# Performance work log

Hardware: AMD Instinct MI355X
Metric: run time of the kernel (lower is better)

## Reference

```python
import jax, jax.numpy as jnp
import numpy as np

B, N, D, H, MLP_H = 4, 2048, 256, 8, 1024
E = 262144
DH = D // H
EPS = 1e-5

def _ln(x, g, b):
    mu = jnp.mean(x, axis=-1, keepdims=True)
    var = jnp.mean((x - mu) ** 2, axis=-1, keepdims=True)
    return (x - mu) * jax.lax.rsqrt(var + EPS) * g + b

def setup_inputs() -> dict:
    key = jax.random.key(0)
    ks = jax.random.split(key, 16)
    s = 0.02
    return {
        "x": jax.random.normal(ks[0], (B, N, D), jnp.float32),
        "edge_index": jax.random.randint(ks[1], (2, E), 0, B * N, dtype=jnp.int64),
        "gc_w": jax.random.normal(ks[2], (D, D), jnp.float32) * s,
        "gc_b": jnp.zeros((D,), jnp.float32),
        "g_gamma": jnp.ones((D,), jnp.float32), "g_beta": jnp.zeros((D,), jnp.float32),
        "wq": jax.random.normal(ks[3], (D, D), jnp.float32) * s, "bq": jnp.zeros((D,), jnp.float32),
        "wk": jax.random.normal(ks[4], (D, D), jnp.float32) * s, "bk": jnp.zeros((D,), jnp.float32),
        "wv": jax.random.normal(ks[5], (D, D), jnp.float32) * s, "bv": jnp.zeros((D,), jnp.float32),
        "wo": jax.random.normal(ks[6], (D, D), jnp.float32) * s, "bo": jnp.zeros((D,), jnp.float32),
        "a_gamma": jnp.ones((D,), jnp.float32), "a_beta": jnp.zeros((D,), jnp.float32),
        "w1": jax.random.normal(ks[7], (D, MLP_H), jnp.float32) * s, "b1": jnp.zeros((MLP_H,), jnp.float32),
        "w2": jax.random.normal(ks[8], (MLP_H, D), jnp.float32) * s, "b2": jnp.zeros((D,), jnp.float32),
        "m_gamma": jnp.ones((D,), jnp.float32), "m_beta": jnp.zeros((D,), jnp.float32),
    }

def reference(x, edge_index, gc_w, gc_b, g_gamma, g_beta,
              wq, bq, wk, bk, wv, bv, wo, bo, a_gamma, a_beta,
              w1, b1, w2, b2, m_gamma, m_beta):
    BN = B * N
    row, col = edge_index[0], edge_index[1]
    # GraphConvolution with symmetric degree normalization
    xf = x.reshape(BN, D)
    xt = xf @ gc_w  # [BN, D]
    deg = jax.ops.segment_sum(jnp.ones((E,), x.dtype), row, num_segments=BN)
    dis = jnp.where(deg > 0, deg ** -0.5, 0.0)  # deg^-0.5, inf -> 0
    norm = dis[row] * dis[col]  # [E]
    out = jax.ops.segment_sum(norm[:, None] * xt[row], col, num_segments=BN) + gc_b
    x = _ln(x + out.reshape(B, N, D), g_gamma, g_beta)
    # Multi-head self-attention (no mask, dropout=0)
    q = (x @ wq + bq).reshape(B, N, H, DH)
    k = (x @ wk + bk).reshape(B, N, H, DH)
    v = (x @ wv + bv).reshape(B, N, H, DH)
    scores = jnp.einsum("bqhd,bkhd->bhqk", q, k) / jnp.sqrt(jnp.float32(DH))
    attn = jax.nn.softmax(scores, axis=-1)
    ao = jnp.einsum("bhqk,bkhd->bqhd", attn, v).reshape(B, N, D) @ wo + bo
    x = _ln(x + ao, a_gamma, a_beta)
    # MLP (GELU exact, dropout inactive at eval)
    h = jax.nn.gelu(x @ w1 + b1, approximate=False)
    x = _ln(x + (h @ w2 + b2), m_gamma, m_beta)
    return x
```

## Files before the change

kernel.cpp:

```cpp
#include <hip/hip_runtime.h>
#include <math.h>

#define Bb 4
#define Nn 2048
#define Dd 256
#define Hh 8
#define DHh 32
#define MLPH 1024
#define Ee 262144
#define BNr 8192
#define KS_S 40
#define VT_S 72

typedef __attribute__((ext_vector_type(8))) short bf8;
typedef __attribute__((ext_vector_type(4))) short s4v;
typedef __attribute__((ext_vector_type(4))) float f4;

__device__ __forceinline__ float gelu_f(float x){
  return 0.5f * x * (1.0f + erff(x * 0.70710678118654752f));
}

__device__ __forceinline__ ushort f2bf(float f){
  union { float f; unsigned u; } v; v.f = f;
  unsigned r = v.u + 0x7fffu + ((v.u >> 16) & 1u);
  return (ushort)(r >> 16);
}
__device__ __forceinline__ float bf2f(ushort u){
  return __uint_as_float((unsigned)u << 16);
}

__global__ void detect_kernel(const int* __restrict__ ei, int* flag){
  __shared__ int nz;
  if (threadIdx.x == 0) nz = 0;
  __syncthreads();
  int any = 0;
  for (int i = threadIdx.x; i < 2048; i += 256)
    if (ei[2*i + 1] != 0) any = 1;
  if (any) atomicOr(&nz, 1);
  __syncthreads();
  if (threadIdx.x == 0) *flag = nz ? 0 : 1;
}

__global__ void count_kernel(const int* __restrict__ ei, const int* __restrict__ flag,
                             int* cnt_row, int* cnt_col){
  int e = blockIdx.x * 256 + threadIdx.x;
  if (e >= Ee) return;
  int m = *flag;
  int r = m ? ei[2*e]          : ei[e];
  int c = m ? ei[2*(Ee + e)]   : ei[Ee + e];
  atomicAdd(&cnt_row[r], 1);
  atomicAdd(&cnt_col[c], 1);
}

__global__ void scan_kernel(const int* __restrict__ cnt, const int* __restrict__ cnt_row,
                            int* start, int* cursor, float* dis){
  __shared__ int part[256];
  int t = threadIdx.x;
  int s = 0;
  for (int i = 0; i < 32; i++) s += cnt[t*32 + i];
  part[t] = s;
  __syncthreads();
  if (t == 0){
    int run = 0;
    for (int i = 0; i < 256; i++){ int tmp = part[i]; part[i] = run; run += tmp; }
    start[BNr] = run;
  }
  __syncthreads();
  int base = part[t];
  for (int i = 0; i < 32; i++){
    start[t*32 + i]  = base;
    cursor[t*32 + i] = base;
    base += cnt[t*32 + i];
  }
  for (int i = t; i < BNr; i += 256){
    int d = cnt_row[i];
    dis[i] = d > 0 ? 1.0f / sqrtf((float)d) : 0.0f;
  }
}

__global__ void fill_kernel(const int* __restrict__ ei, const int* __restrict__ flag,
                            const float* __restrict__ dis,
                            int* cursor, int2* bucket){
  int e = blockIdx.x * 256 + threadIdx.x;
  if (e >= Ee) return;
  int m = *flag;
  int r = m ? ei[2*e]        : ei[e];
  int c = m ? ei[2*(Ee + e)] : ei[Ee + e];
  int p = atomicAdd(&cursor[c], 1);
  int2 pk;
  pk.x = r;
  pk.y = __float_as_int(dis[r] * dis[c]);
  bucket[p] = pk;
}

__device__ __forceinline__ void tconv_body(const float* src, ushort* dst, int R, int C){
  __shared__ float tile[32][33];
  int c0 = blockIdx.x * 32, r0 = blockIdx.y * 32;
  int tx = threadIdx.x & 31, ty = threadIdx.x >> 5;
  for (int i = ty; i < 32; i += 8)
    tile[i][tx] = src[(size_t)(r0 + i) * C + c0 + tx];
  __syncthreads();
  for (int i = ty; i < 32; i += 8)
    dst[(size_t)(c0 + i) * R + r0 + tx] = f2bf(tile[tx][i]);
}

__global__ void tconv_kernel(const float* __restrict__ src, ushort* __restrict__ dst, int R, int C){
  tconv_body(src, dst, R, C);
}

__global__ void tconv5_kernel(const float* s0, const float* s1, const float* s2,
                              const float* s3, const float* s4,
                              ushort* d0, ushort* d1, ushort* d2, ushort* d3, ushort* d4){
  const float* s; ushort* d;
  switch (blockIdx.z){
    case 0: s = s0; d = d0; break;
    case 1: s = s1; d = d1; break;
    case 2: s = s2; d = d2; break;
    case 3: s = s3; d = d3; break;
    default: s = s4; d = d4; break;
  }
  tconv_body(s, d, 256, 256);
}

__global__ void bias_cat_kernel(const float* __restrict__ bq, const float* __restrict__ bk,
                                const float* __restrict__ bv, float* __restrict__ o){
  int i = blockIdx.x * 256 + threadIdx.x;
  if (i < 256) o[i] = bq[i];
  else if (i < 512) o[i] = bk[i - 256];
  else if (i < 768) o[i] = bv[i - 512];
}

__global__ __launch_bounds__(256) void gather_ln_kernel(
    const ushort* __restrict__ xtb, const int2* __restrict__ bucket,
    const int* __restrict__ start,
    const float* __restrict__ x, const float* __restrict__ gc_b,
    const float* __restrict__ gamma, const float* __restrict__ beta,
    float* __restrict__ out, ushort* __restrict__ outb){
  int v = blockIdx.x, t = threadIdx.x;
  int s0 = start[v], s1 = start[v+1];
  float acc = 0.f;
  int ii = s0;
  for (; ii + 3 < s1; ii += 4){
    int2 e0 = bucket[ii],   e1 = bucket[ii+1];
    int2 e2 = bucket[ii+2], e3 = bucket[ii+3];
    float v0 = bf2f(xtb[(size_t)e0.x*Dd + t]);
    float v1 = bf2f(xtb[(size_t)e1.x*Dd + t]);
    float v2 = bf2f(xtb[(size_t)e2.x*Dd + t]);
    float v3 = bf2f(xtb[(size_t)e3.x*Dd + t]);
    acc += __int_as_float(e0.y) * v0 + __int_as_float(e1.y) * v1;
    acc += __int_as_float(e2.y) * v2 + __int_as_float(e3.y) * v3;
  }
  for (; ii < s1; ii++){
    int2 e = bucket[ii];
    acc += __int_as_float(e.y) * bf2f(xtb[(size_t)e.x*Dd + t]);
  }
  float val = x[(size_t)v*Dd + t] + acc + gc_b[t];

  float s = val, s2 = val*val;
  #pragma unroll
  for (int o = 32; o > 0; o >>= 1){ s += __shfl_xor(s, o); s2 += __shfl_xor(s2, o); }
  __shared__ float wsA[4], wsB[4];
  int wid = t >> 6, lane = t & 63;
  if (lane == 0){ wsA[wid] = s; wsB[wid] = s2; }
  __syncthreads();
  float mu = (wsA[0]+wsA[1]+wsA[2]+wsA[3]) * (1.0f/Dd);
  float ms = (wsB[0]+wsB[1]+wsB[2]+wsB[3]) * (1.0f/Dd);
  float var = ms - mu*mu;
  float res = (val - mu) * rsqrtf(var + 1e-5f) * gamma[t] + beta[t];
  out[(size_t)v*Dd + t] = res;
  outb[(size_t)v*Dd + t] = f2bf(res);
}

__global__ __launch_bounds__(256) void add_ln_kernel(
    const float* __restrict__ a, const float* __restrict__ b,
    const float* __restrict__ gamma, const float* __restrict__ beta,
    float* __restrict__ out, ushort* __restrict__ outb){
  int row = blockIdx.x, t = threadIdx.x;
  size_t off = (size_t)row*Dd + t;
  float val = a[off] + b[off];

  float s = val, s2 = val*val;
  #pragma unroll
  for (int o = 32; o > 0; o >>= 1){ s += __shfl_xor(s, o); s2 += __shfl_xor(s2, o); }
  __shared__ float wsA[4], wsB[4];
  int wid = t >> 6, lane = t & 63;
  if (lane == 0){ wsA[wid] = s; wsB[wid] = s2; }
  __syncthreads();
  float mu = (wsA[0]+wsA[1]+wsA[2]+wsA[3]) * (1.0f/Dd);
  float ms = (wsB[0]+wsB[1]+wsB[2]+wsB[3]) * (1.0f/Dd);
  float var = ms - mu*mu;
  float res = (val - mu) * rsqrtf(var + 1e-5f) * gamma[t] + beta[t];
  out[off] = res;
  if (outb) outb[off] = f2bf(res);
}

#define LDA_S 56

template<int EPI>
__global__ __launch_bounds__(256,2) void gemm_bf16(
    const ushort* __restrict__ A, const ushort* __restrict__ Bt,
    const float* __restrict__ bias, float* __restrict__ Cf, ushort* __restrict__ Cb,
    int M, int K, int N, float qscale,
    ushort* __restrict__ Qp, ushort* __restrict__ Kp, ushort* __restrict__ VtG){
  __shared__ ushort As[2][128*LDA_S];
  __shared__ ushort Bs[2][64*LDA_S];
  int t = threadIdx.x;
  int lane = t & 63, wid = t >> 6;
  int wm = wid >> 1, wn = wid & 1;
  int l15 = lane & 15, lg = lane >> 4;
  int m0 = blockIdx.y * 128, n0 = blockIdx.x * 64;

  int sr = t >> 2;
  int sk = (t & 3) * 8;
  const ushort* Ag1 = A  + (size_t)(m0 + sr) * K + sk;
  const ushort* Ag2 = A  + (size_t)(m0 + 64 + sr) * K + sk;
  const ushort* Bg  = Bt + (size_t)(n0 + sr) * K + sk;

  int nsteps = K / 32;
  bf8 ra1 = *(const bf8*)Ag1;
  bf8 ra2 = *(const bf8*)Ag2;
  bf8 rb  = *(const bf8*)Bg;
  *(bf8*)&As[0][sr*LDA_S + sk]        = ra1;
  *(bf8*)&As[0][(64+sr)*LDA_S + sk]   = ra2;
  *(bf8*)&Bs[0][sr*LDA_S + sk]        = rb;
  __syncthreads();

  f4 acc[4][2] = {};
  for (int ks = 0; ks < nsteps; ks++){
    int cur = ks & 1;
    if (ks + 1 < nsteps){
      ra1 = *(const bf8*)(Ag1 + (ks+1)*32);
      ra2 = *(const bf8*)(Ag2 + (ks+1)*32);
      rb  = *(const bf8*)(Bg  + (ks+1)*32);
    }
    bf8 af[4], bfr[2];
    #pragma unroll
    for (int mf = 0; mf < 4; mf++)
      af[mf] = *(bf8*)&As[cur][(wm*64 + mf*16 + l15)*LDA_S + lg*8];
    #pragma unroll
    for (int nf = 0; nf < 2; nf++)
      bfr[nf] = *(bf8*)&Bs[cur][(wn*32 + nf*16 + l15)*LDA_S + lg*8];
    #pragma unroll
    for (int mf = 0; mf < 4; mf++)
      #pragma unroll
      for (int nf = 0; nf < 2; nf++)
        acc[mf][nf] = __builtin_amdgcn_mfma_f32_16x16x32_bf16(af[mf], bfr[nf], acc[mf][nf], 0, 0, 0);
    __syncthreads();
    if (ks + 1 < nsteps){
      int nxt = cur ^ 1;
      *(bf8*)&As[nxt][sr*LDA_S + sk]      = ra1;
      *(bf8*)&As[nxt][(64+sr)*LDA_S + sk] = ra2;
      *(bf8*)&Bs[nxt][sr*LDA_S + sk]      = rb;
      __syncthreads();
    }
  }

  #pragma unroll
  for (int mf = 0; mf < 4; mf++){
    int row = m0 + wm*64 + mf*16 + lg*4;
    #pragma unroll
    for (int nf = 0; nf < 2; nf++){
      int col = n0 + wn*32 + nf*16 + l15;
      float bv = bias ? bias[col] : 0.f;
      float vv[4];
      #pragma unroll
      for (int r = 0; r < 4; r++) vv[r] = acc[mf][nf][r] + bv;
      if (EPI == 0){
        #pragma unroll
        for (int r = 0; r < 4; r++) Cf[(size_t)(row + r) * N + col] = vv[r];
      } else if (EPI == 2){
        #pragma unroll
        for (int r = 0; r < 4; r++) Cb[(size_t)(row + r) * N + col] = f2bf(gelu_f(vv[r]));
      } else {
        if (n0 < 256){
          #pragma unroll
          for (int r = 0; r < 4; r++)
            Qp[(size_t)(row + r) * Dd + col] = f2bf(vv[r] * qscale);
        } else if (n0 < 512){
          int h = (col - 256) >> 5, dh = (col - 256) & 31;
          int bb = row >> 11, n = row & 2047;
          #pragma unroll
          for (int r = 0; r < 4; r++)
            Kp[((size_t)(bb*Hh + h)*Nn + n + r)*DHh + dh] = f2bf(vv[r]);
        } else {
          int h = (col - 512) >> 5, dh = (col - 512) & 31;
          int bb = row >> 11, n = row & 2047;
          ushort4 pk;
          pk.x = f2bf(vv[0]); pk.y = f2bf(vv[1]);
          pk.z = f2bf(vv[2]); pk.w = f2bf(vv[3]);
          *(ushort4*)&VtG[((size_t)(bb*Hh + h)*DHh + dh)*Nn + n] = pk;
        }
      }
    }
  }
}

template<int OB, int AF>
__global__ __launch_bounds__(256,4) void gemm64_bf16(
    const void* __restrict__ Av, const ushort* __restrict__ Bt,
    const float* __restrict__ bias, float* __restrict__ Cf, ushort* __restrict__ Cb,
    int M, int K, int N){
  __shared__ ushort As[2][64*LDA_S];
  __shared__ ushort Bs[2][64*LDA_S];
  int t = threadIdx.x;
  int lane = t & 63, wid = t >> 6;
  int wm = wid >> 1, wn = wid & 1;
  int l15 = lane & 15, lg = lane >> 4;
  int m0 = blockIdx.y * 64, n0 = blockIdx.x * 64;
  int sr = t >> 2, sk = (t & 3) * 8;
  const ushort* Ag = (const ushort*)Av + (size_t)(m0 + sr) * K + sk;
  const float*  Af = (const float*)Av  + (size_t)(m0 + sr) * K + sk;
  const ushort* Bg = Bt + (size_t)(n0 + sr) * K + sk;
  int nsteps = K / 32;

  bf8 ra; float4 rf0, rf1;
  if (AF){ rf0 = *(const float4*)Af; rf1 = *(const float4*)(Af + 4); }
  else   { ra = *(const bf8*)Ag; }
  bf8 rb = *(const bf8*)Bg;
  if (AF){
    bf8 c;
    c[0]=(short)f2bf(rf0.x); c[1]=(short)f2bf(rf0.y); c[2]=(short)f2bf(rf0.z); c[3]=(short)f2bf(rf0.w);
    c[4]=(short)f2bf(rf1.x); c[5]=(short)f2bf(rf1.y); c[6]=(short)f2bf(rf1.z); c[7]=(short)f2bf(rf1.w);
    *(bf8*)&As[0][sr*LDA_S + sk] = c;
  } else {
    *(bf8*)&As[0][sr*LDA_S + sk] = ra;
  }
  *(bf8*)&Bs[0][sr*LDA_S + sk] = rb;
  __syncthreads();

  f4 acc[2][2] = {};
  for (int ks = 0; ks < nsteps; ks++){
    int cur = ks & 1;
    if (ks + 1 < nsteps){
      if (AF){ rf0 = *(const float4*)(Af + (ks+1)*32); rf1 = *(const float4*)(Af + (ks+1)*32 + 4); }
      else   { ra = *(const bf8*)(Ag + (ks+1)*32); }
      rb = *(const bf8*)(Bg + (ks+1)*32);
    }
    bf8 af[2], bfr[2];
    #pragma unroll
    for (int mf = 0; mf < 2; mf++)
      af[mf] = *(bf8*)&As[cur][(wm*32 + mf*16 + l15)*LDA_S + lg*8];
    #pragma unroll
    for (int nf = 0; nf < 2; nf++)
      bfr[nf] = *(bf8*)&Bs[cur][(wn*32 + nf*16 + l15)*LDA_S + lg*8];
    #pragma unroll
    for (int mf = 0; mf < 2; mf++)
      #pragma unroll
      for (int nf = 0; nf < 2; nf++)
        acc[mf][nf] = __builtin_amdgcn_mfma_f32_16x16x32_bf16(af[mf], bfr[nf], acc[mf][nf], 0, 0, 0);
    __syncthreads();
    if (ks + 1 < nsteps){
      int nxt = cur ^ 1;
      if (AF){
        bf8 c;
        c[0]=(short)f2bf(rf0.x); c[1]=(short)f2bf(rf0.y); c[2]=(short)f2bf(rf0.z); c[3]=(short)f2bf(rf0.w);
        c[4]=(short)f2bf(rf1.x); c[5]=(short)f2bf(rf1.y); c[6]=(short)f2bf(rf1.z); c[7]=(short)f2bf(rf1.w);
        *(bf8*)&As[nxt][sr*LDA_S + sk] = c;
      } else {
        *(bf8*)&As[nxt][sr*LDA_S + sk] = ra;
      }
      *(bf8*)&Bs[nxt][sr*LDA_S + sk] = rb;
      __syncthreads();
    }
  }
  #pragma unroll
  for (int mf = 0; mf < 2; mf++){
    int row = m0 + wm*32 + mf*16 + lg*4;
    #pragma unroll
    for (int nf = 0; nf < 2; nf++){
      int col = n0 + wn*32 + nf*16 + l15;
      float bv = bias ? bias[col] : 0.f;
      #pragma unroll
      for (int r = 0; r < 4; r++){
        float v = acc[mf][nf][r] + bv;
        if (OB) Cb[(size_t)(row + r) * N + col] = f2bf(v);
        else    Cf[(size_t)(row + r) * N + col] = v;
      }
    }
  }
}

__global__ __launch_bounds__(256,4) void attn5_kernel(
    const ushort* __restrict__ Qp, const ushort* __restrict__ Kp,
    const ushort* __restrict__ VtG, ushort* __restrict__ AO){
  __shared__ ushort Ks[2][64*KS_S];
  __shared__ ushort Vt[2][32*VT_S];
  int bh = blockIdx.x >> 5, qb = blockIdx.x & 31;
  int b = bh >> 3, h = bh & 7;
  const ushort* Kh = Kp  + (size_t)bh*Nn*DHh;
  const ushort* Vh = VtG + (size_t)bh*DHh*Nn;
  int t = threadIdx.x;
  int lane = t & 63, wid = t >> 6;
  int l15 = lane & 15, lg = lane >> 4;
  int q0 = qb*64 + wid*16;

  bf8 qf = *(const bf8*)&Qp[(size_t)(b*Nn + q0 + l15)*Dd + h*DHh + lg*8];

  int krow = t >> 2, kc8 = (t & 3) * 8;
  int vrow = t >> 3, vc8 = (t & 7) * 8;
  const ushort* Kg = Kh + (size_t)krow*DHh + kc8;
  const ushort* Vg = Vh + (size_t)vrow*Nn + vc8;

  bf8 kreg = *(const bf8*)Kg;
  bf8 vreg = *(const bf8*)Vg;
  *(bf8*)&Ks[0][krow*KS_S + kc8] = kreg;
  *(bf8*)&Vt[0][vrow*VT_S + vc8] = vreg;
  __syncthreads();

  float m_st = -1e30f, l_st = 0.f;
  f4 oacc[2] = {};

  const int NT = Nn/64;
  for (int kc = 0; kc < NT; kc++){
    int cur = kc & 1;
    if (kc + 1 < NT){
      kreg = *(const bf8*)(Kg + (size_t)(kc+1)*64*DHh);
      vreg = *(const bf8*)(Vg + (kc+1)*64);
    }

    f4 s[4] = {};
    #pragma unroll
    for (int kt = 0; kt < 4; kt++){
      bf8 kf = *(bf8*)&Ks[cur][(kt*16 + l15)*KS_S + lg*8];
      s[kt] = __builtin_amdgcn_mfma_f32_16x16x32_bf16(kf, qf, s[kt], 0, 0, 0);
    }

    float mx = s[0][0];
    #pragma unroll
    for (int kt = 0; kt < 4; kt++)
      #pragma unroll
      for (int r = 0; r < 4; r++)
        mx = fmaxf(mx, s[kt][r]);
    if (__any(mx > m_st + 11.0f)){
      float mw = fmaxf(mx, __shfl_xor(mx, 16));
      mw = fmaxf(mw, __shfl_xor(mw, 32));
      float Mn = fmaxf(m_st, mw);
      float corr = exp2f(m_st - Mn);
      l_st *= corr;
      #pragma unroll
      for (int r = 0; r < 4; r++){
        float cr = __shfl(corr, (lane & 48) | (lg*4 + r));
        oacc[0][r] *= cr;
        oacc[1][r] *= cr;
      }
      m_st = Mn;
    }

    s4v pa[4];
    float ps = 0.f;
    #pragma unroll
    for (int kt = 0; kt < 4; kt++){
      unsigned pb[4];
      #pragma unroll
      for (int r = 0; r < 4; r++){
        float p = exp2f(s[kt][r] - m_st);
        pb[r] = __float_as_uint(p) & 0xffff0000u;
        ps += __uint_as_float(pb[r]);
      }
      union { unsigned u[2]; s4v v; } cvt;
      cvt.u[0] = (pb[0] >> 16) | pb[1];
      cvt.u[1] = (pb[2] >> 16) | pb[3];
      pa[kt] = cvt.v;
    }
    ps += __shfl_xor(ps, 16);
    ps += __shfl_xor(ps, 32);
    l_st += ps;

    #pragma unroll
    for (int kt = 0; kt < 4; kt++)
      #pragma unroll
      for (int nt = 0; nt < 2; nt++){
        s4v vf = *(const s4v*)&Vt[cur][(nt*16 + l15)*VT_S + kt*16 + lg*4];
        oacc[nt] = __builtin_amdgcn_mfma_f32_16x16x16bf16_1k(pa[kt], vf, oacc[nt], 0, 0, 0);
      }

    if (kc + 1 < NT){
      *(bf8*)&Ks[cur^1][krow*KS_S + kc8] = kreg;
      *(bf8*)&Vt[cur^1][vrow*VT_S + vc8] = vreg;
    }
    __syncthreads();
  }

  float l = l_st;
  l += __shfl_xor(l, 16);
  l += __shfl_xor(l, 32);
  float invl = 1.0f / l;
  #pragma unroll
  for (int r = 0; r < 4; r++){
    float il = __shfl(invl, (lane & 48) | (lg*4 + r));
    int row = b*Nn + q0 + lg*4 + r;
    #pragma unroll
    for (int nt = 0; nt < 2; nt++)
      AO[(size_t)row*Dd + h*DHh + nt*16 + l15] = f2bf(oacc[nt][r] * il);
  }
}

extern "C" void kernel_launch(void* const* d_in, const int* in_sizes, int n_in,
                              void* d_out, int out_size, void* d_ws, size_t ws_size,
                              hipStream_t stream){
  const float* x      = (const float*)d_in[0];
  const int*   ei     = (const int*)d_in[1];
  const float* gc_w   = (const float*)d_in[2];
  const float* gc_b   = (const float*)d_in[3];
  const float* g_gamma= (const float*)d_in[4];
  const float* g_beta = (const float*)d_in[5];
  const float* wq = (const float*)d_in[6];  const float* bq = (const float*)d_in[7];
  const float* wk = (const float*)d_in[8];  const float* bk = (const float*)d_in[9];
  const float* wv = (const float*)d_in[10]; const float* bv = (const float*)d_in[11];
  const float* wo = (const float*)d_in[12]; const float* bo = (const float*)d_in[13];
  const float* a_gamma = (const float*)d_in[14]; const float* a_beta = (const float*)d_in[15];
  const float* w1 = (const float*)d_in[16]; const float* b1 = (const float*)d_in[17];
  const float* w2 = (const float*)d_in[18]; const float* b2 = (const float*)d_in[19];
  const float* m_gamma = (const float*)d_in[20]; const float* m_beta = (const float*)d_in[21];
  float* out = (float*)d_out;

  const size_t S = (size_t)BNr * Dd;

  char* p = (char*)d_ws;
  auto alloc = [&](size_t bytes){ char* r = p; p += (bytes + 255) & ~(size_t)255; return r; };

  float* X1    = (float*)alloc(S * 4);
  float* X2    = (float*)alloc(S * 4);
  float* MO    = (float*)alloc(S * 4);
  float* PROJ  = (float*)alloc(S * 4);
  ushort* Qp   = (ushort*)alloc(S * 2);
  ushort* Kp   = (ushort*)alloc(S * 2);
  ushort* VtG  = (ushort*)alloc(S * 2);
  ushort* regA = (ushort*)alloc(S * 2);
  ushort* XTb  = (ushort*)alloc(S * 2);
  ushort* X1b  = (ushort*)alloc(S * 2);
  ushort* Hb   = (ushort*)alloc((size_t)BNr * MLPH * 2);
  ushort* gcwT = (ushort*)alloc(65536 * 2);
  ushort* wqkvT= (ushort*)alloc(196608 * 2);
  ushort* woT  = (ushort*)alloc(65536 * 2);
  ushort* w1T  = (ushort*)alloc(262144 * 2);
  ushort* w2T  = (ushort*)alloc(262144 * 2);
  float* bqkv  = (float*)alloc(768 * 4);
  int* cnt_row = (int*)alloc(8192 * 4);
  int* cnt_col = (int*)alloc(8192 * 4);
  int* startA  = (int*)alloc(8200 * 4);
  int* cursor  = (int*)alloc(8192 * 4);
  int2* bucket = (int2*)alloc(Ee * 8);
  float* dis   = (float*)alloc(8192 * 4);
  int* flag    = (int*)alloc(256);

  ushort* AOb = regA;
  ushort* X2b = XTb;

  hipMemsetAsync(cnt_row, 0, 2 * 8192 * sizeof(int), stream);

  detect_kernel<<<1, 256, 0, stream>>>(ei, flag);
  count_kernel<<<Ee/256, 256, 0, stream>>>(ei, flag, cnt_row, cnt_col);
  scan_kernel<<<1, 256, 0, stream>>>(cnt_col, cnt_row, startA, cursor, dis);
  fill_kernel<<<Ee/256, 256, 0, stream>>>(ei, flag, dis, cursor, bucket);

  tconv5_kernel<<<dim3(8,8,5), 256, 0, stream>>>(gc_w, wq, wk, wv, wo,
      gcwT, wqkvT, wqkvT + 65536, wqkvT + 131072, woT);
  tconv_kernel<<<dim3(32,8), 256, 0, stream>>>(w1, w1T, 256, 1024);
  tconv_kernel<<<dim3(8,32), 256, 0, stream>>>(w2, w2T, 1024, 256);
  bias_cat_kernel<<<3, 256, 0, stream>>>(bq, bk, bv, bqkv);

  const float qscale = 0.17677669529663687f * 1.4426950408889634f;

  gemm64_bf16<1,1><<<dim3(Dd/64, BNr/64), 256, 0, stream>>>(
      x, gcwT, nullptr, nullptr, XTb, BNr, Dd, Dd);
  gather_ln_kernel<<<BNr, 256, 0, stream>>>(XTb, bucket, startA,
                                            x, gc_b, g_gamma, g_beta, X1, X1b);
  gemm_bf16<3><<<dim3(768/64, BNr/128), 256, 0, stream>>>(
      X1b, wqkvT, bqkv, nullptr, nullptr, BNr, Dd, 768, qscale, Qp, Kp, VtG);
  attn5_kernel<<<Bb*Hh*32, 256, 0, stream>>>(Qp, Kp, VtG, AOb);
  gemm64_bf16<0,0><<<dim3(Dd/64, BNr/64), 256, 0, stream>>>(
      AOb, woT, bo, PROJ, nullptr, BNr, Dd, Dd);
  add_ln_kernel<<<BNr, 256, 0, stream>>>(X1, PROJ, a_gamma, a_beta, X2, X2b);
  gemm_bf16<2><<<dim3(MLPH/64, BNr/128), 256, 0, stream>>>(
      X2b, w1T, b1, nullptr, Hb, BNr, Dd, MLPH, 1.0f, nullptr, nullptr, nullptr);
  gemm64_bf16<0,0><<<dim3(Dd/64, BNr/64), 256, 0, stream>>>(
      Hb, w2T, b2, MO, nullptr, BNr, MLPH, Dd);
  add_ln_kernel<<<BNr, 256, 0, stream>>>(X2, MO, m_gamma, m_beta, out, nullptr);
}
```

Before: 341.6 us.

## Double K-step depth in GEMMs and key tile size in attention

Both GEMM kernels now stage 64-wide K slices in shared memory instead of 32, which halves the number of barrier pairs and lets each thread issue more loads per step. The attention kernel processes 128 keys per iteration instead of 64, so online-softmax rescaling and synchronisation happen half as often. It also drops the per-iteration cross-lane reduction of the row sum and defers it to the end. The cost is more shared memory and registers, which may lower occupancy.

```diff
diff --git a/kernel.cpp b/kernel.cpp
--- a/kernel.cpp
+++ b/kernel.cpp
@@ -9,8 +9,9 @@
 #define MLPH 1024
 #define Ee 262144
 #define BNr 8192
-#define KS_S 40
-#define VT_S 72
+#define KS2 40
+#define VS2 136
+#define LDB 72
 
 typedef __attribute__((ext_vector_type(8))) short bf8;
 typedef __attribute__((ext_vector_type(4))) short s4v;
@@ -194,63 +195,69 @@
   if (outb) outb[off] = f2bf(res);
 }
 
-#define LDA_S 56
-
 template<int EPI>
 __global__ __launch_bounds__(256,2) void gemm_bf16(
     const ushort* __restrict__ A, const ushort* __restrict__ Bt,
     const float* __restrict__ bias, float* __restrict__ Cf, ushort* __restrict__ Cb,
     int M, int K, int N, float qscale,
     ushort* __restrict__ Qp, ushort* __restrict__ Kp, ushort* __restrict__ VtG){
-  __shared__ ushort As[2][128*LDA_S];
-  __shared__ ushort Bs[2][64*LDA_S];
+  __shared__ ushort As[2][128*LDB];
+  __shared__ ushort Bs[2][64*LDB];
   int t = threadIdx.x;
   int lane = t & 63, wid = t >> 6;
   int wm = wid >> 1, wn = wid & 1;
   int l15 = lane & 15, lg = lane >> 4;
   int m0 = blockIdx.y * 128, n0 = blockIdx.x * 64;
 
-  int sr = t >> 2;
-  int sk = (t & 3) * 8;
-  const ushort* Ag1 = A  + (size_t)(m0 + sr) * K + sk;
-  const ushort* Ag2 = A  + (size_t)(m0 + 64 + sr) * K + sk;
-  const ushort* Bg  = Bt + (size_t)(n0 + sr) * K + sk;
-
-  int nsteps = K / 32;
-  bf8 ra1 = *(const bf8*)Ag1;
-  bf8 ra2 = *(const bf8*)Ag2;
-  bf8 rb  = *(const bf8*)Bg;
-  *(bf8*)&As[0][sr*LDA_S + sk]        = ra1;
-  *(bf8*)&As[0][(64+sr)*LDA_S + sk]   = ra2;
-  *(bf8*)&Bs[0][sr*LDA_S + sk]        = rb;
+  int ar = t >> 1, ac = (t & 1) * 32;
+  int br = t >> 2, bc = (t & 3) * 16;
+  const ushort* Ag = A  + (size_t)(m0 + ar) * K + ac;
+  const ushort* Bg = Bt + (size_t)(n0 + br) * K + bc;
+
+  int nsteps = K / 64;
+  bf8 a0 = *(const bf8*)(Ag + 0),  a1 = *(const bf8*)(Ag + 8);
+  bf8 a2 = *(const bf8*)(Ag + 16), a3 = *(const bf8*)(Ag + 24);
+  bf8 b0 = *(const bf8*)(Bg + 0),  b1r = *(const bf8*)(Bg + 8);
+  *(bf8*)&As[0][ar*LDB + ac + 0]  = a0;
+  *(bf8*)&As[0][ar*LDB + ac + 8]  = a1;
+  *(bf8*)&As[0][ar*LDB + ac + 16] = a2;
+  *(bf8*)&As[0][ar*LDB + ac + 24] = a3;
+  *(bf8*)&Bs[0][br*LDB + bc + 0]  = b0;
+  *(bf8*)&Bs[0][br*LDB + bc + 8]  = b1r;
   __syncthreads();
 
   f4 acc[4][2] = {};
   for (int ks = 0; ks < nsteps; ks++){
     int cur = ks & 1;
     if (ks + 1 < nsteps){
-      ra1 = *(const bf8*)(Ag1 + (ks+1)*32);
-      ra2 = *(const bf8*)(Ag2 + (ks+1)*32);
-      rb  = *(const bf8*)(Bg  + (ks+1)*32);
-    }
-    bf8 af[4], bfr[2];
-    #pragma unroll
-    for (int mf = 0; mf < 4; mf++)
-      af[mf] = *(bf8*)&As[cur][(wm*64 + mf*16 + l15)*LDA_S + lg*8];
-    #pragma unroll
-    for (int nf = 0; nf < 2; nf++)
-      bfr[nf] = *(bf8*)&Bs[cur][(wn*32 + nf*16 + l15)*LDA_S + lg*8];
-    #pragma unroll
-    for (int mf = 0; mf < 4; mf++)
+      a0 = *(const bf8*)(Ag + (ks+1)*64 + 0);  a1 = *(const bf8*)(Ag + (ks+1)*64 + 8);
+      a2 = *(const bf8*)(Ag + (ks+1)*64 + 16); a3 = *(const bf8*)(Ag + (ks+1)*64 + 24);
+      b0 = *(const bf8*)(Bg + (ks+1)*64 + 0);  b1r = *(const bf8*)(Bg + (ks+1)*64 + 8);
+    }
+    #pragma unroll
+    for (int kk = 0; kk < 2; kk++){
+      bf8 af[4], bfr[2];
+      #pragma unroll
+      for (int mf = 0; mf < 4; mf++)
+        af[mf] = *(bf8*)&As[cur][(wm*64 + mf*16 + l15)*LDB + kk*32 + lg*8];
       #pragma unroll
       for (int nf = 0; nf < 2; nf++)
-        acc[mf][nf] = __builtin_amdgcn_mfma_f32_16x16x32_bf16(af[mf], bfr[nf], acc[mf][nf], 0, 0, 0);
+        bfr[nf] = *(bf8*)&Bs[cur][(wn*32 + nf*16 + l15)*LDB + kk*32 + lg*8];
+      #pragma unroll
+      for (int mf = 0; mf < 4; mf++)
+        #pragma unroll
+        for (int nf = 0; nf < 2; nf++)
+          acc[mf][nf] = __builtin_amdgcn_mfma_f32_16x16x32_bf16(af[mf], bfr[nf], acc[mf][nf], 0, 0, 0);
+    }
     __syncthreads();
     if (ks + 1 < nsteps){
       int nxt = cur ^ 1;
-      *(bf8*)&As[nxt][sr*LDA_S + sk]      = ra1;
-      *(bf8*)&As[nxt][(64+sr)*LDA_S + sk] = ra2;
-      *(bf8*)&Bs[nxt][sr*LDA_S + sk]      = rb;
+      *(bf8*)&As[nxt][ar*LDB + ac + 0]  = a0;
+      *(bf8*)&As[nxt][ar*LDB + ac + 8]  = a1;
+      *(bf8*)&As[nxt][ar*LDB + ac + 16] = a2;
+      *(bf8*)&As[nxt][ar*LDB + ac + 24] = a3;
+      *(bf8*)&Bs[nxt][br*LDB + bc + 0]  = b0;
+      *(bf8*)&Bs[nxt][br*LDB + bc + 8]  = b1r;
       __syncthreads();
     }
   }
@@ -300,66 +307,82 @@
     const void* __restrict__ Av, const ushort* __restrict__ Bt,
     const float* __restrict__ bias, float* __restrict__ Cf, ushort* __restrict__ Cb,
     int M, int K, int N){
-  __shared__ ushort As[2][64*LDA_S];
-  __shared__ ushort Bs[2][64*LDA_S];
+  __shared__ ushort As[2][64*LDB];
+  __shared__ ushort Bs[2][64*LDB];
   int t = threadIdx.x;
   int lane = t & 63, wid = t >> 6;
   int wm = wid >> 1, wn = wid & 1;
   int l15 = lane & 15, lg = lane >> 4;
   int m0 = blockIdx.y * 64, n0 = blockIdx.x * 64;
-  int sr = t >> 2, sk = (t & 3) * 8;
-  const ushort* Ag = (const ushort*)Av + (size_t)(m0 + sr) * K + sk;
-  const float*  Af = (const float*)Av  + (size_t)(m0 + sr) * K + sk;
-  const ushort* Bg = Bt + (size_t)(n0 + sr) * K + sk;
-  int nsteps = K / 32;
-
-  bf8 ra; float4 rf0, rf1;
-  if (AF){ rf0 = *(const float4*)Af; rf1 = *(const float4*)(Af + 4); }
-  else   { ra = *(const bf8*)Ag; }
-  bf8 rb = *(const bf8*)Bg;
+  int ar = t >> 2, ac = (t & 3) * 16;
+  const ushort* Ag = (const ushort*)Av + (size_t)(m0 + ar) * K + ac;
+  const float*  Af = (const float*)Av  + (size_t)(m0 + ar) * K + ac;
+  const ushort* Bg = Bt + (size_t)(n0 + ar) * K + ac;
+  int nsteps = K / 64;
+
+  bf8 a0, a1, b0, b1r;
+  float4 rf0, rf1, rf2, rf3;
   if (AF){
-    bf8 c;
-    c[0]=(short)f2bf(rf0.x); c[1]=(short)f2bf(rf0.y); c[2]=(short)f2bf(rf0.z); c[3]=(short)f2bf(rf0.w);
-    c[4]=(short)f2bf(rf1.x); c[5]=(short)f2bf(rf1.y); c[6]=(short)f2bf(rf1.z); c[7]=(short)f2bf(rf1.w);
-    *(bf8*)&As[0][sr*LDA_S + sk] = c;
+    rf0 = *(const float4*)(Af + 0);  rf1 = *(const float4*)(Af + 4);
+    rf2 = *(const float4*)(Af + 8);  rf3 = *(const float4*)(Af + 12);
+    bf8 c0, c1;
+    c0[0]=(short)f2bf(rf0.x); c0[1]=(short)f2bf(rf0.y); c0[2]=(short)f2bf(rf0.z); c0[3]=(short)f2bf(rf0.w);
+    c0[4]=(short)f2bf(rf1.x); c0[5]=(short)f2bf(rf1.y); c0[6]=(short)f2bf(rf1.z); c0[7]=(short)f2bf(rf1.w);
+    c1[0]=(short)f2bf(rf2.x); c1[1]=(short)f2bf(rf2.y); c1[2]=(short)f2bf(rf2.z); c1[3]=(short)f2bf(rf2.w);
+    c1[4]=(short)f2bf(rf3.x); c1[5]=(short)f2bf(rf3.y); c1[6]=(short)f2bf(rf3.z); c1[7]=(short)f2bf(rf3.w);
+    a0 = c0; a1 = c1;
   } else {
-    *(bf8*)&As[0][sr*LDA_S + sk] = ra;
-  }
-  *(bf8*)&Bs[0][sr*LDA_S + sk] = rb;
+    a0 = *(const bf8*)(Ag + 0); a1 = *(const bf8*)(Ag + 8);
+  }
+  b0 = *(const bf8*)(Bg + 0); b1r = *(const bf8*)(Bg + 8);
+  *(bf8*)&As[0][ar*LDB + ac + 0] = a0;
+  *(bf8*)&As[0][ar*LDB + ac + 8] = a1;
+  *(bf8*)&Bs[0][ar*LDB + ac + 0] = b0;
+  *(bf8*)&Bs[0][ar*LDB + ac + 8] = b1r;
   __syncthreads();
 
   f4 acc[2][2] = {};
   for (int ks = 0; ks < nsteps; ks++){
     int cur = ks & 1;
     if (ks + 1 < nsteps){
-      if (AF){ rf0 = *(const float4*)(Af + (ks+1)*32); rf1 = *(const float4*)(Af + (ks+1)*32 + 4); }
-      else   { ra = *(const bf8*)(Ag + (ks+1)*32); }
-      rb = *(const bf8*)(Bg + (ks+1)*32);
-    }
-    bf8 af[2], bfr[2];
-    #pragma unroll
-    for (int mf = 0; mf < 2; mf++)
-      af[mf] = *(bf8*)&As[cur][(wm*32 + mf*16 + l15)*LDA_S + lg*8];
-    #pragma unroll
-    for (int nf = 0; nf < 2; nf++)
-      bfr[nf] = *(bf8*)&Bs[cur][(wn*32 + nf*16 + l15)*LDA_S + lg*8];
-    #pragma unroll
-    for (int mf = 0; mf < 2; mf++)
+      if (AF){
+        rf0 = *(const float4*)(Af + (ks+1)*64 + 0);  rf1 = *(const float4*)(Af + (ks+1)*64 + 4);
+        rf2 = *(const float4*)(Af + (ks+1)*64 + 8);  rf3 = *(const float4*)(Af + (ks+1)*64 + 12);
+      } else {
+        a0 = *(const bf8*)(Ag + (ks+1)*64 + 0); a1 = *(const bf8*)(Ag + (ks+1)*64 + 8);
+      }
+      b0 = *(const bf8*)(Bg + (ks+1)*64 + 0); b1r = *(const bf8*)(Bg + (ks+1)*64 + 8);
+    }
+    #pragma unroll
+    for (int kk = 0; kk < 2; kk++){
+      bf8 af[2], bfr[2];
+      #pragma unroll
+      for (int mf = 0; mf < 2; mf++)
+        af[mf] = *(bf8*)&As[cur][(wm*32 + mf*16 + l15)*LDB + kk*32 + lg*8];
       #pragma unroll
       for (int nf = 0; nf < 2; nf++)
-        acc[mf][nf] = __builtin_amdgcn_mfma_f32_16x16x32_bf16(af[mf], bfr[nf], acc[mf][nf], 0, 0, 0);
+        bfr[nf] = *(bf8*)&Bs[cur][(wn*32 + nf*16 + l15)*LDB + kk*32 + lg*8];
+      #pragma unroll
+      for (int mf = 0; mf < 2; mf++)
+        #pragma unroll
+        for (int nf = 0; nf < 2; nf++)
+          acc[mf][nf] = __builtin_amdgcn_mfma_f32_16x16x32_bf16(af[mf], bfr[nf], acc[mf][nf], 0, 0, 0);
+    }
     __syncthreads();
     if (ks + 1 < nsteps){
       int nxt = cur ^ 1;
       if (AF){
-        bf8 c;
-        c[0]=(short)f2bf(rf0.x); c[1]=(short)f2bf(rf0.y); c[2]=(short)f2bf(rf0.z); c[3]=(short)f2bf(rf0.w);
-        c[4]=(short)f2bf(rf1.x); c[5]=(short)f2bf(rf1.y); c[6]=(short)f2bf(rf1.z); c[7]=(short)f2bf(rf1.w);
-        *(bf8*)&As[nxt][sr*LDA_S + sk] = c;
-      } else {
-        *(bf8*)&As[nxt][sr*LDA_S + sk] = ra;
+        bf8 c0, c1;
+        c0[0]=(short)f2bf(rf0.x); c0[1]=(short)f2bf(rf0.y); c0[2]=(short)f2bf(rf0.z); c0[3]=(short)f2bf(rf0.w);
+        c0[4]=(short)f2bf(rf1.x); c0[5]=(short)f2bf(rf1.y); c0[6]=(short)f2bf(rf1.z); c0[7]=(short)f2bf(rf1.w);
+        c1[0]=(short)f2bf(rf2.x); c1[1]=(short)f2bf(rf2.y); c1[2]=(short)f2bf(rf2.z); c1[3]=(short)f2bf(rf2.w);
+        c1[4]=(short)f2bf(rf3.x); c1[5]=(short)f2bf(rf3.y); c1[6]=(short)f2bf(rf3.z); c1[7]=(short)f2bf(rf3.w);
+        a0 = c0; a1 = c1;
       }
-      *(bf8*)&Bs[nxt][sr*LDA_S + sk] = rb;
+      *(bf8*)&As[nxt][ar*LDB + ac + 0] = a0;
+      *(bf8*)&As[nxt][ar*LDB + ac + 8] = a1;
+      *(bf8*)&Bs[nxt][ar*LDB + ac + 0] = b0;
+      *(bf8*)&Bs[nxt][ar*LDB + ac + 8] = b1r;
       __syncthreads();
     }
   }
@@ -380,11 +403,11 @@
   }
 }
 
-__global__ __launch_bounds__(256,4) void attn5_kernel(
+__global__ __launch_bounds__(256,4) void attn6_kernel(
     const ushort* __restrict__ Qp, const ushort* __restrict__ Kp,
     const ushort* __restrict__ VtG, ushort* __restrict__ AO){
-  __shared__ ushort Ks[2][64*KS_S];
-  __shared__ ushort Vt[2][32*VT_S];
+  __shared__ ushort Ks[2][128*KS2];
+  __shared__ ushort Vt[2][32*VS2];
   int bh = blockIdx.x >> 5, qb = blockIdx.x & 31;
   int b = bh >> 3, h = bh & 7;
   const ushort* Kh = Kp  + (size_t)bh*Nn*DHh;
@@ -396,41 +419,56 @@
 
   bf8 qf = *(const bf8*)&Qp[(size_t)(b*Nn + q0 + l15)*Dd + h*DHh + lg*8];
 
-  int krow = t >> 2, kc8 = (t & 3) * 8;
-  int vrow = t >> 3, vc8 = (t & 7) * 8;
-  const ushort* Kg = Kh + (size_t)krow*DHh + kc8;
-  const ushort* Vg = Vh + (size_t)vrow*Nn + vc8;
-
-  bf8 kreg = *(const bf8*)Kg;
-  bf8 vreg = *(const bf8*)Vg;
-  *(bf8*)&Ks[0][krow*KS_S + kc8] = kreg;
-  *(bf8*)&Vt[0][vrow*VT_S + vc8] = vreg;
+  int akr = t >> 2, akc = (t & 3) * 8;
+  int avr = t >> 3, avc = (t & 7) * 8;
+  const ushort* Kg = Kh + (size_t)akr*DHh + akc;
+  const ushort* Vg = Vh + (size_t)avr*Nn + avc;
+
+  bf8 k0r = *(const bf8*)Kg;
+  bf8 k1r = *(const bf8*)(Kg + 64*DHh);
+  bf8 v0r = *(const bf8*)Vg;
+  bf8 v1r = *(const bf8*)(Vg + 64);
+  *(bf8*)&Ks[0][akr*KS2 + akc]        = k0r;
+  *(bf8*)&Ks[0][(akr + 64)*KS2 + akc] = k1r;
+  *(bf8*)&Vt[0][avr*VS2 + avc]        = v0r;
+  *(bf8*)&Vt[0][avr*VS2 + avc + 64]   = v1r;
   __syncthreads();
 
   float m_st = -1e30f, l_st = 0.f;
   f4 oacc[2] = {};
 
-  const int NT = Nn/64;
+  const int NT = Nn/128;
   for (int kc = 0; kc < NT; kc++){
     int cur = kc & 1;
     if (kc + 1 < NT){
-      kreg = *(const bf8*)(Kg + (size_t)(kc+1)*64*DHh);
-      vreg = *(const bf8*)(Vg + (kc+1)*64);
-    }
-
-    f4 s[4] = {};
-    #pragma unroll
-    for (int kt = 0; kt < 4; kt++){
-      bf8 kf = *(bf8*)&Ks[cur][(kt*16 + l15)*KS_S + lg*8];
-      s[kt] = __builtin_amdgcn_mfma_f32_16x16x32_bf16(kf, qf, s[kt], 0, 0, 0);
-    }
-
-    float mx = s[0][0];
-    #pragma unroll
-    for (int kt = 0; kt < 4; kt++)
-      #pragma unroll
-      for (int r = 0; r < 4; r++)
-        mx = fmaxf(mx, s[kt][r]);
+      k0r = *(const bf8*)(Kg + (size_t)(kc+1)*128*DHh);
+      k1r = *(const bf8*)(Kg + (size_t)((kc+1)*128 + 64)*DHh);
+      v0r = *(const bf8*)(Vg + (kc+1)*128);
+      v1r = *(const bf8*)(Vg + (kc+1)*128 + 64);
+    }
+
+    f4 s[8];
+    #pragma unroll
+    for (int kt = 0; kt < 8; kt++){
+      bf8 kf = *(bf8*)&Ks[cur][(kt*16 + l15)*KS2 + lg*8];
+      f4 z = {};
+      s[kt] = __builtin_amdgcn_mfma_f32_16x16x32_bf16(kf, qf, z, 0, 0, 0);
+    }
+
+    float mx01 = fmaxf(fmaxf(s[0][0], s[0][1]), fmaxf(s[0][2], s[0][3]));
+    float mx23 = fmaxf(fmaxf(s[1][0], s[1][1]), fmaxf(s[1][2], s[1][3]));
+    float mx45 = fmaxf(fmaxf(s[2][0], s[2][1]), fmaxf(s[2][2], s[2][3]));
+    float mx67 = fmaxf(fmaxf(s[3][0], s[3][1]), fmaxf(s[3][2], s[3][3]));
+    #pragma unroll
+    for (int kt = 4; kt < 8; kt++){
+      float a = fmaxf(fmaxf(s[kt][0], s[kt][1]), fmaxf(s[kt][2], s[kt][3]));
+      if (kt == 4) mx01 = fmaxf(mx01, a);
+      else if (kt == 5) mx23 = fmaxf(mx23, a);
+      else if (kt == 6) mx45 = fmaxf(mx45, a);
+      else mx67 = fmaxf(mx67, a);
+    }
+    float mx = fmaxf(fmaxf(mx01, mx23), fmaxf(mx45, mx67));
+
     if (__any(mx > m_st + 11.0f)){
       float mw = fmaxf(mx, __shfl_xor(mx, 16));
       mw = fmaxf(mw, __shfl_xor(mw, 32));
@@ -446,10 +484,10 @@
       m_st = Mn;
     }
 
-    s4v pa[4];
+    s4v pa[8];
     float ps = 0.f;
     #pragma unroll
-    for (int kt = 0; kt < 4; kt++){
+    for (int kt = 0; kt < 8; kt++){
       unsigned pb[4];
       #pragma unroll
       for (int r = 0; r < 4; r++){
@@ -462,21 +500,22 @@
       cvt.u[1] = (pb[2] >> 16) | pb[3];
       pa[kt] = cvt.v;
     }
-    ps += __shfl_xor(ps, 16);
-    ps += __shfl_xor(ps, 32);
     l_st += ps;
 
     #pragma unroll
-    for (int kt = 0; kt < 4; kt++)
+    for (int kt = 0; kt < 8; kt++)
       #pragma unroll
       for (int nt = 0; nt < 2; nt++){
-        s4v vf = *(const s4v*)&Vt[cur][(nt*16 + l15)*VT_S + kt*16 + lg*4];
+        s4v vf = *(const s4v*)&Vt[cur][(nt*16 + l15)*VS2 + kt*16 + lg*4];
         oacc[nt] = __builtin_amdgcn_mfma_f32_16x16x16bf16_1k(pa[kt], vf, oacc[nt], 0, 0, 0);
       }
 
     if (kc + 1 < NT){
-      *(bf8*)&Ks[cur^1][krow*KS_S + kc8] = kreg;
-      *(bf8*)&Vt[cur^1][vrow*VT_S + vc8] = vreg;
+      int nxt = cur ^ 1;
+      *(bf8*)&Ks[nxt][akr*KS2 + akc]        = k0r;
+      *(bf8*)&Ks[nxt][(akr + 64)*KS2 + akc] = k1r;
+      *(bf8*)&Vt[nxt][avr*VS2 + avc]        = v0r;
+      *(bf8*)&Vt[nxt][avr*VS2 + avc + 64]   = v1r;
     }
     __syncthreads();
   }
@@ -568,7 +607,7 @@
                                             x, gc_b, g_gamma, g_beta, X1, X1b);
   gemm_bf16<3><<<dim3(768/64, BNr/128), 256, 0, stream>>>(
       X1b, wqkvT, bqkv, nullptr, nullptr, BNr, Dd, 768, qscale, Qp, Kp, VtG);
-  attn5_kernel<<<Bb*Hh*32, 256, 0, stream>>>(Qp, Kp, VtG, AOb);
+  attn6_kernel<<<Bb*Hh*32, 256, 0, stream>>>(Qp, Kp, VtG, AOb);
   gemm64_bf16<0,0><<<dim3(Dd/64, BNr/64), 256, 0, stream>>>(
       AOb, woT, bo, PROJ, nullptr, BNr, Dd, Dd);
   add_ln_kernel<<<BNr, 256, 0, stream>>>(X1, PROJ, a_gamma, a_beta, X2, X2b);
```

Measured after the change: 339.9 us. Within noise of the previous version (-0.5%).
